# Optimization experiments

Hardware: AMD Instinct MI355X
Metric: run time of the kernel (lower is better)

## Reference

```python
import jax, jax.numpy as jnp
import numpy as np

B, L, D = 2, 4096, 768
H, HD = 12, 64
EPS = 1e-6


def setup_inputs() -> dict:
    key = jax.random.key(0)
    ks = jax.random.split(key, 5)
    x = jax.random.normal(ks[0], (B, L, D), dtype=jnp.float32)
    # realistic rope tables
    inv_freq = 1.0 / (10000.0 ** (np.arange(0, HD, 2, dtype=np.float32) / HD))
    t = np.arange(L, dtype=np.float32)
    freqs = np.outer(t, inv_freq)  # (L, HD/2)
    emb = np.concatenate([freqs, freqs], axis=-1)  # (L, HD)
    rope_cos = jnp.asarray(np.cos(emb))
    rope_sin = jnp.asarray(np.sin(emb))
    Wqkv = jax.random.normal(ks[1], (3 * D, D), dtype=jnp.float32) * (1.0 / np.sqrt(D))
    Wout = jax.random.normal(ks[2], (D, D), dtype=jnp.float32) * (1.0 / np.sqrt(D))
    q_norm_w = jnp.ones((HD,), dtype=jnp.float32)
    k_norm_w = jnp.ones((HD,), dtype=jnp.float32)
    return {"x": x, "rope_cos": rope_cos, "rope_sin": rope_sin,
            "Wqkv": Wqkv, "Wout": Wout,
            "q_norm_w": q_norm_w, "k_norm_w": k_norm_w}


def _rms_norm(x, w):
    # x: (..., HD); computed in float32 like the torch module
    norm = jax.lax.rsqrt(jnp.mean(jnp.square(x.astype(jnp.float32)), axis=-1, keepdims=True) + EPS)
    return (x.astype(jnp.float32) * norm).astype(x.dtype) * w


def _rotate_half(x):
    x1, x2 = jnp.split(x, 2, axis=-1)
    return jnp.concatenate([-x2, x1], axis=-1)


def reference(x, rope_cos, rope_sin, Wqkv, Wout, q_norm_w, k_norm_w):
    b, l, d = x.shape
    # fused QKV projection (Linear with no bias): x @ Wqkv.T
    qkv = jnp.einsum('bld,ed->ble', x, Wqkv).reshape(b, l, 3, H, HD)
    q, k, v = qkv[:, :, 0], qkv[:, :, 1], qkv[:, :, 2]  # (B, L, H, HD)
    q = jnp.transpose(q, (0, 2, 1, 3))  # (B, H, L, HD)
    k = jnp.transpose(k, (0, 2, 1, 3))
    v = jnp.transpose(v, (0, 2, 1, 3))
    # per-head RMSNorm on q and k
    q = _rms_norm(q, q_norm_w)
    k = _rms_norm(k, k_norm_w)
    # RoPE: cos/sin (L, HD) broadcast over (B, H)
    cos = rope_cos[None, None, :, :]
    sin = rope_sin[None, None, :, :]
    q = q * cos + _rotate_half(q) * sin
    k = k * cos + _rotate_half(k) * sin
    # scaled dot product attention (no mask)
    scale = 1.0 / jnp.sqrt(jnp.asarray(HD, dtype=q.dtype))
    scores = jnp.einsum('bhqd,bhkd->bhqk', q, k) * scale  # (B, H, L, L)
    attn = jax.nn.softmax(scores, axis=-1)
    out = jnp.einsum('bhqk,bhkd->bhqd', attn, v)  # (B, H, L, HD)
    out = jnp.transpose(out, (0, 2, 1, 3)).reshape(b, l, d)
    return jnp.einsum('bld,ed->ble', out, Wout)
```

## Files before the change

kernel.cpp:

```cpp
#include <hip/hip_runtime.h>
#include <hip/hip_bf16.h>

typedef float f32x4 __attribute__((ext_vector_type(4)));
typedef float f32x16 __attribute__((ext_vector_type(16)));
typedef short bf16x8 __attribute__((ext_vector_type(8)));
typedef unsigned short ushort8_t __attribute__((ext_vector_type(8)));

#define L_SEQ 4096
#define DMODEL 768
#define NHEAD 12
#define HDIM 64
#define QSCALE (0.125f * 1.44269504f)

__device__ __forceinline__ unsigned short f2bf(float f) {
    __hip_bfloat16 h = __float2bfloat16(f);
    return *reinterpret_cast<unsigned short*>(&h);
}

__device__ __forceinline__ unsigned pack2bf(float a, float b) {
    unsigned r;
    asm("v_cvt_pk_bf16_f32 %0, %1, %2" : "=v"(r) : "v"(a), "v"(b));
    return r;
}

__device__ __forceinline__ void gload16(const void* g, void* l) {
    __builtin_amdgcn_global_load_lds(
        (const __attribute__((address_space(1))) unsigned int*)g,
        (__attribute__((address_space(3))) unsigned int*)l, 16, 0, 0);
}

__global__ __launch_bounds__(256) void cvt3_f32_bf16(
    const float* __restrict__ a, unsigned short* __restrict__ oa, int na,
    const float* __restrict__ bsrc, unsigned short* __restrict__ ob, int nb,
    const float* __restrict__ csrc, unsigned short* __restrict__ oc, int nc)
{
    int i = (blockIdx.x * 256 + threadIdx.x) * 4;
    const float* in; unsigned short* out;
    if (i < na) { in = a; out = oa; }
    else if (i < na + nb) { in = bsrc; out = ob; i -= na; }
    else if (i < na + nb + nc) { in = csrc; out = oc; i -= na + nb; }
    else return;
    float4 v = *reinterpret_cast<const float4*>(in + i);
    ushort4 o;
    o.x = f2bf(v.x); o.y = f2bf(v.y); o.z = f2bf(v.z); o.w = f2bf(v.w);
    *reinterpret_cast<ushort4*>(out + i) = o;
}

#define BM 128
#define BN 128
#define BKK 64

__global__ __launch_bounds__(256) void gemm_qkv_fused(
    const unsigned short* __restrict__ A, const unsigned short* __restrict__ Bt,
    const float* __restrict__ cosb, const float* __restrict__ sinb,
    const float* __restrict__ qw, const float* __restrict__ kw,
    unsigned short* __restrict__ Qb, unsigned short* __restrict__ Kb,
    unsigned short* __restrict__ Vt)
{
    __shared__ union SM {
        struct { unsigned short As[BM][BKK]; unsigned short Bs[BN][BKK]; } st;
        unsigned short ep[4][64][72];
    } sm;

    const int K = DMODEL;
    const int tid  = threadIdx.x;
    const int lane = tid & 63;
    const int wid  = tid >> 6;
    const int r = lane & 15, g = lane >> 4;
    const int wr = wid >> 1, wc = wid & 1;
    const int m0 = blockIdx.y * BM;
    const int n0 = blockIdx.x * BN;

    f32x4 acc[4][4];
    for (int i = 0; i < 4; ++i)
        for (int j = 0; j < 4; ++j)
            acc[i][j] = (f32x4){0.f, 0.f, 0.f, 0.f};

    for (int kt = 0; kt < K; kt += BKK) {
        __syncthreads();
        for (int p = 0; p < 4; ++p) {
            int idx = wid * 64 + p * 256 + lane;
            int row = idx >> 3;
            int ch  = (idx & 7) * 8;
            gload16(&A[(size_t)(m0 + row) * K + kt + ch],
                    (char*)sm.st.As + (size_t)(wid * 64 + p * 256) * 16);
            gload16(&Bt[(size_t)(n0 + row) * K + kt + ch],
                    (char*)sm.st.Bs + (size_t)(wid * 64 + p * 256) * 16);
        }
        __syncthreads();
        for (int k0 = 0; k0 < BKK; k0 += 32) {
            bf16x8 a[4], b[4];
            for (int i = 0; i < 4; ++i)
                a[i] = *reinterpret_cast<const bf16x8*>(&sm.st.As[wr * 64 + i * 16 + r][k0 + 8 * g]);
            for (int j = 0; j < 4; ++j)
                b[j] = *reinterpret_cast<const bf16x8*>(&sm.st.Bs[wc * 64 + j * 16 + r][k0 + 8 * g]);
            for (int i = 0; i < 4; ++i)
                for (int j = 0; j < 4; ++j)
                    acc[i][j] = __builtin_amdgcn_mfma_f32_16x16x32_bf16(a[i], b[j], acc[i][j], 0, 0, 0);
        }
    }

    __syncthreads();

    const int e0  = n0 + wc * 64;
    const int sec = e0 / DMODEL;
    const int h   = (e0 % DMODEL) / HDIM;
    const int row0 = m0 + wr * 64;
    const int b   = row0 >> 12;
    const int l0  = row0 & (L_SEQ - 1);
    unsigned short (*ep)[72] = sm.ep[wid];

    if (sec < 2) {
        const float* nw = (sec == 0) ? qw : kw;
        float wv[4];
        for (int j = 0; j < 4; ++j) wv[j] = nw[j * 16 + r];
        for (int i = 0; i < 4; ++i) {
            for (int t = 0; t < 4; ++t) {
                float ss = acc[i][0][t] * acc[i][0][t] + acc[i][1][t] * acc[i][1][t]
                         + acc[i][2][t] * acc[i][2][t] + acc[i][3][t] * acc[i][3][t];
                ss += __shfl_xor(ss, 1);
                ss += __shfl_xor(ss, 2);
                ss += __shfl_xor(ss, 4);
                ss += __shfl_xor(ss, 8);
                float inv = rsqrtf(ss * (1.f / 64.f) + 1e-6f);
                int lr = i * 16 + 4 * g + t;
                int l  = l0 + lr;
                float qn[4];
                for (int j = 0; j < 4; ++j) qn[j] = acc[i][j][t] * inv * wv[j];
                for (int j = 0; j < 4; ++j) {
                    int d = j * 16 + r;
                    float c = cosb[l * HDIM + d], s = sinb[l * HDIM + d];
                    float sgn = (j < 2) ? -1.f : 1.f;
                    float res = qn[j] * c + sgn * qn[j ^ 2] * s;
                    if (sec == 0) res *= QSCALE;
                    ep[lr][d] = f2bf(res);
                }
            }
        }
        unsigned short* dst = ((sec == 0) ? Qb : Kb)
            + ((size_t)(b * NHEAD + h) * L_SEQ + l0) * HDIM;
        for (int it = 0; it < 8; ++it) {
            int idx = it * 64 + lane;
            int lr = idx >> 3, ch = (idx & 7) * 8;
            ushort8_t v = *reinterpret_cast<const ushort8_t*>(&ep[lr][ch]);
            *reinterpret_cast<ushort8_t*>(&dst[(size_t)lr * HDIM + ch]) = v;
        }
    } else {
        for (int i = 0; i < 4; ++i)
            for (int t = 0; t < 4; ++t) {
                int lr = i * 16 + 4 * g + t;
                for (int j = 0; j < 4; ++j)
                    ep[j * 16 + r][lr] = f2bf(acc[i][j][t]);
            }
        unsigned short* dst = Vt + ((size_t)(b * NHEAD + h) * HDIM) * L_SEQ + l0;
        for (int it = 0; it < 8; ++it) {
            int idx = it * 64 + lane;
            int d = idx >> 3, ch = (idx & 7) * 8;
            ushort8_t v = *reinterpret_cast<const ushort8_t*>(&ep[d][ch]);
            *reinterpret_cast<ushort8_t*>(&dst[(size_t)d * L_SEQ + ch]) = v;
        }
    }
}

__global__ __launch_bounds__(256) void gemm_bf16_nt(
    const unsigned short* __restrict__ A, const unsigned short* __restrict__ Bt,
    float* __restrict__ C, int M, int N, int K)
{
    __shared__ unsigned short As[BM][BKK];
    __shared__ unsigned short Bs[BN][BKK];
    const int tid  = threadIdx.x;
    const int lane = tid & 63;
    const int wid  = tid >> 6;
    const int r = lane & 15, g = lane >> 4;
    const int wr = wid >> 1, wc = wid & 1;
    const int m0 = blockIdx.y * BM;
    const int n0 = blockIdx.x * BN;

    f32x4 acc[4][4];
    for (int i = 0; i < 4; ++i)
        for (int j = 0; j < 4; ++j)
            acc[i][j] = (f32x4){0.f, 0.f, 0.f, 0.f};

    for (int kt = 0; kt < K; kt += BKK) {
        __syncthreads();
        for (int p = 0; p < 4; ++p) {
            int idx = wid * 64 + p * 256 + lane;
            int row = idx >> 3;
            int ch  = (idx & 7) * 8;
            gload16(&A[(size_t)(m0 + row) * K + kt + ch],
                    (char*)As + (size_t)(wid * 64 + p * 256) * 16);
            gload16(&Bt[(size_t)(n0 + row) * K + kt + ch],
                    (char*)Bs + (size_t)(wid * 64 + p * 256) * 16);
        }
        __syncthreads();
        for (int k0 = 0; k0 < BKK; k0 += 32) {
            bf16x8 a[4], b[4];
            for (int i = 0; i < 4; ++i)
                a[i] = *reinterpret_cast<const bf16x8*>(&As[wr * 64 + i * 16 + r][k0 + 8 * g]);
            for (int j = 0; j < 4; ++j)
                b[j] = *reinterpret_cast<const bf16x8*>(&Bs[wc * 64 + j * 16 + r][k0 + 8 * g]);
            for (int i = 0; i < 4; ++i)
                for (int j = 0; j < 4; ++j)
                    acc[i][j] = __builtin_amdgcn_mfma_f32_16x16x32_bf16(a[i], b[j], acc[i][j], 0, 0, 0);
        }
    }
    for (int i = 0; i < 4; ++i)
        for (int j = 0; j < 4; ++j)
            for (int t = 0; t < 4; ++t) {
                int row = m0 + wr * 64 + i * 16 + 4 * g + t;
                int col = n0 + wc * 64 + j * 16 + r;
                C[(size_t)row * N + col] = acc[i][j][t];
            }
}

__global__ __launch_bounds__(256, 3) void flashattn(
    const unsigned short* __restrict__ Qb, const unsigned short* __restrict__ Kb,
    const unsigned short* __restrict__ Vt, unsigned short* __restrict__ aob)
{
    __shared__ unsigned short Ksm[2][64 * 64];
    __shared__ unsigned short Vsm[2][64 * 64];

    const int lin = blockIdx.x;
    const int bh = (lin & 7) + 8 * (lin >> 8);
    const int qblk = (lin >> 3) & 31;
    const int b = bh / NHEAD, h = bh % NHEAD;
    const int tid = threadIdx.x;
    const int wid = tid >> 6, lane = tid & 63;
    const int l31 = lane & 31, half = lane >> 5;
    const int q0 = qblk * 128 + wid * 32;

    bf16x8 qf[4];
    {
        const unsigned short* Qp = Qb + ((size_t)bh * L_SEQ + q0 + l31) * HDIM + 8 * half;
        for (int dt = 0; dt < 4; ++dt)
            qf[dt] = *reinterpret_cast<const bf16x8*>(Qp + dt * 16);
    }

    const unsigned short* Kbase = Kb + (size_t)bh * L_SEQ * HDIM;
    const unsigned short* Vbase = Vt + (size_t)bh * HDIM * L_SEQ;

    const int row0 = tid >> 3;
    const int c0 = ((tid & 7) * 16) ^ ((row0 & 7) << 4);
    const char* kp0 = (const char*)(Kbase + (size_t)row0 * HDIM) + c0;
    const char* vp0 = (const char*)(Vbase + (size_t)row0 * L_SEQ) + c0;

    f32x16 o0, o1, sA0, sA1, sB0, sB1;
    for (int e = 0; e < 16; ++e) {
        o0[e] = 0.f; o1[e] = 0.f;
        sA0[e] = 0.f; sA1[e] = 0.f; sB0[e] = 0.f; sB1[e] = 0.f;
    }
    float lacc = 0.f;

    auto stageK = [&](int buf, int t) {
        size_t off = (size_t)t * (64 * HDIM * 2);
        gload16(kp0 + off, (char*)Ksm[buf] + wid * 1024);
        gload16(kp0 + off + 32 * HDIM * 2, (char*)Ksm[buf] + wid * 1024 + 4096);
    };
    auto stageV = [&](int buf, int t) {
        size_t off = (size_t)t * 128;
        gload16(vp0 + off, (char*)Vsm[buf] + wid * 1024);
        gload16(vp0 + off + (size_t)32 * L_SEQ * 2, (char*)Vsm[buf] + wid * 1024 + 4096);
    };

    auto qk = [&](f32x16& s0, f32x16& s1, const unsigned short* Kbuf) {
        const char* rp0 = (const char*)Kbuf + l31 * 128;
        const char* rp1 = rp0 + 32 * 128;
        const int sw = (l31 & 7) << 4;
        for (int dt = 0; dt < 4; ++dt) {
            int co = (dt * 32 + half * 16) ^ sw;
            bf16x8 kf0 = *reinterpret_cast<const bf16x8*>(rp0 + co);
            bf16x8 kf1 = *reinterpret_cast<const bf16x8*>(rp1 + co);
            s0 = __builtin_amdgcn_mfma_f32_32x32x16_bf16(kf0, qf[dt], s0, 0, 0, 0);
            s1 = __builtin_amdgcn_mfma_f32_32x32x16_bf16(kf1, qf[dt], s1, 0, 0, 0);
        }
    };

    auto softmax_pa = [&](f32x16& s0, f32x16& s1, bf16x8* pa) {
        float ts = 0.f;
        for (int kh = 0; kh < 2; ++kh) {
            f32x16& s = kh ? s1 : s0;
            for (int kk = 0; kk < 2; ++kk) {
                float p8[8];
                for (int e = 0; e < 8; ++e) p8[e] = __builtin_amdgcn_exp2f(s[8 * kk + e]);
                float t0 = (p8[0] + p8[1]) + (p8[2] + p8[3]);
                float t1 = (p8[4] + p8[5]) + (p8[6] + p8[7]);
                ts += t0 + t1;
                unsigned A = pack2bf(p8[0], p8[1]);
                unsigned Bp = pack2bf(p8[2], p8[3]);
                unsigned C = pack2bf(p8[4], p8[5]);
                unsigned D = pack2bf(p8[6], p8[7]);
                asm("v_permlane32_swap_b32 %0, %1" : "+v"(A), "+v"(C));
                asm("v_permlane32_swap_b32 %0, %1" : "+v"(Bp), "+v"(D));
                union { unsigned u[4]; bf16x8 v; } tt;
                tt.u[0] = A; tt.u[1] = Bp; tt.u[2] = C; tt.u[3] = D;
                pa[2 * kh + kk] = tt.v;
            }
            for (int e = 0; e < 16; ++e) s[e] = 0.f;
        }
        lacc += ts;
    };

    auto pv = [&](const bf16x8* pa, const unsigned short* Vbuf) {
        const char* rp0 = (const char*)Vbuf + l31 * 128;
        const char* rp1 = rp0 + 32 * 128;
        const int sw = (l31 & 7) << 4;
        for (int kt = 0; kt < 4; ++kt) {
            int co = (kt * 32 + half * 16) ^ sw;
            bf16x8 vf0 = *reinterpret_cast<const bf16x8*>(rp0 + co);
            bf16x8 vf1 = *reinterpret_cast<const bf16x8*>(rp1 + co);
            o0 = __builtin_amdgcn_mfma_f32_32x32x16_bf16(pa[kt], vf0, o0, 0, 0, 0);
            o1 = __builtin_amdgcn_mfma_f32_32x32x16_bf16(pa[kt], vf1, o1, 0, 0, 0);
        }
    };

    stageK(0, 0);
    __syncthreads();
    stageK(1, 1); stageV(0, 0);
    __builtin_amdgcn_s_setprio(1);
    qk(sA0, sA1, Ksm[0]);
    __builtin_amdgcn_s_setprio(0);
    __syncthreads();

    bf16x8 pa[4];
    for (int i = 0; i < 31; ++i) {
        int t1 = 2 * i + 1;
        stageK(0, t1 + 1); stageV(1, t1);
        __builtin_amdgcn_s_setprio(1);
        qk(sB0, sB1, Ksm[1]);
        softmax_pa(sA0, sA1, pa);
        pv(pa, Vsm[0]);
        __builtin_amdgcn_s_setprio(0);
        __syncthreads();
        int t2 = t1 + 1;
        stageK(1, t2 + 1); stageV(0, t2);
        __builtin_amdgcn_s_setprio(1);
        qk(sA0, sA1, Ksm[0]);
        softmax_pa(sB0, sB1, pa);
        pv(pa, Vsm[1]);
        __builtin_amdgcn_s_setprio(0);
        __syncthreads();
    }
    stageV(1, 63);
    __builtin_amdgcn_s_setprio(1);
    qk(sB0, sB1, Ksm[1]);
    softmax_pa(sA0, sA1, pa);
    pv(pa, Vsm[0]);
    __builtin_amdgcn_s_setprio(0);
    __syncthreads();
    softmax_pa(sB0, sB1, pa);
    pv(pa, Vsm[1]);

    float ltot = lacc + __shfl_xor(lacc, 32);

    for (int j = 0; j < 16; ++j) {
        int q = (j & 3) + 8 * (j >> 2) + 4 * half;
        float linv = 1.f / __shfl(ltot, q);
        size_t base = ((size_t)(b * L_SEQ + q0 + q)) * DMODEL + h * HDIM + l31;
        aob[base] = f2bf(o0[j] * linv);
        aob[base + 32] = f2bf(o1[j] * linv);
    }
}

extern "C" void kernel_launch(void* const* d_in, const int* in_sizes, int n_in,
                              void* d_out, int out_size, void* d_ws, size_t ws_size,
                              hipStream_t stream) {
    const float* x        = (const float*)d_in[0];
    const float* rope_cos = (const float*)d_in[1];
    const float* rope_sin = (const float*)d_in[2];
    const float* Wqkv     = (const float*)d_in[3];
    const float* Wout     = (const float*)d_in[4];
    const float* q_norm_w = (const float*)d_in[5];
    const float* k_norm_w = (const float*)d_in[6];
    float* out = (float*)d_out;

    const int BL = 2 * L_SEQ;
    const int nx    = BL * DMODEL;
    const int nwqkv = 3 * DMODEL * DMODEL;
    const int nwout = DMODEL * DMODEL;

    char* w = (char*)d_ws;
    unsigned short* xb    = (unsigned short*)w; w += (size_t)nx * 2;
    unsigned short* wqkvb = (unsigned short*)w; w += (size_t)nwqkv * 2;
    unsigned short* woutb = (unsigned short*)w; w += (size_t)nwout * 2;
    unsigned short* Qb    = (unsigned short*)w; w += (size_t)nx * 2;
    unsigned short* Kb    = (unsigned short*)w; w += (size_t)nx * 2;
    unsigned short* Vtb   = (unsigned short*)w; w += (size_t)nx * 2;
    unsigned short* aob   = (unsigned short*)w; w += (size_t)nx * 2;

    {
        int total = (nx + nwqkv + nwout) / 4;
        cvt3_f32_bf16<<<(total + 255) / 256, 256, 0, stream>>>(
            x, xb, nx, Wqkv, wqkvb, nwqkv, Wout, woutb, nwout);
    }

    {
        dim3 grid(3 * DMODEL / BN, BL / BM);
        gemm_qkv_fused<<<grid, 256, 0, stream>>>(xb, wqkvb, rope_cos, rope_sin,
                                                 q_norm_w, k_norm_w, Qb, Kb, Vtb);
    }

    flashattn<<<768, 256, 0, stream>>>(Qb, Kb, Vtb, aob);

    {
        dim3 grid(DMODEL / BN, BL / BM);
        gemm_bf16_nt<<<grid, 256, 0, stream>>>(aob, woutb, out, BL, DMODEL, DMODEL);
    }
}
```

Measured before the change: 209.9 us.

## Replace software-pipelined QK/softmax/PV loop with simple double-buffered loop

Removes the cross-iteration software pipeline, in which QK for tile t+1 was computed while softmax and PV of tile t ran, using two sets of score accumulators. It replaces it with a straightforward loop: prefetch K/V for the next tile, then QK, softmax and PV on the current tile. This frees 32 accumulator registers per lane, which could raise occupancy. In exchange it loses the overlap of MFMA work with exp/softmax work inside a wave. The setprio scope also changes so softmax runs at normal priority.

```diff
diff --git a/kernel.cpp b/kernel.cpp
--- a/kernel.cpp
+++ b/kernel.cpp
@@ -244,10 +244,9 @@
     const char* kp0 = (const char*)(Kbase + (size_t)row0 * HDIM) + c0;
     const char* vp0 = (const char*)(Vbase + (size_t)row0 * L_SEQ) + c0;
 
-    f32x16 o0, o1, sA0, sA1, sB0, sB1;
+    f32x16 o0, o1, s0, s1;
     for (int e = 0; e < 16; ++e) {
-        o0[e] = 0.f; o1[e] = 0.f;
-        sA0[e] = 0.f; sA1[e] = 0.f; sB0[e] = 0.f; sB1[e] = 0.f;
+        o0[e] = 0.f; o1[e] = 0.f; s0[e] = 0.f; s1[e] = 0.f;
     }
     float lacc = 0.f;
 
@@ -262,7 +261,7 @@
         gload16(vp0 + off + (size_t)32 * L_SEQ * 2, (char*)Vsm[buf] + wid * 1024 + 4096);
     };
 
-    auto qk = [&](f32x16& s0, f32x16& s1, const unsigned short* Kbuf) {
+    auto qk = [&](const unsigned short* Kbuf) {
         const char* rp0 = (const char*)Kbuf + l31 * 128;
         const char* rp1 = rp0 + 32 * 128;
         const int sw = (l31 & 7) << 4;
@@ -275,16 +274,14 @@
         }
     };
 
-    auto softmax_pa = [&](f32x16& s0, f32x16& s1, bf16x8* pa) {
+    auto softmax_pa = [&](bf16x8* pa) {
         float ts = 0.f;
         for (int kh = 0; kh < 2; ++kh) {
             f32x16& s = kh ? s1 : s0;
             for (int kk = 0; kk < 2; ++kk) {
                 float p8[8];
                 for (int e = 0; e < 8; ++e) p8[e] = __builtin_amdgcn_exp2f(s[8 * kk + e]);
-                float t0 = (p8[0] + p8[1]) + (p8[2] + p8[3]);
-                float t1 = (p8[4] + p8[5]) + (p8[6] + p8[7]);
-                ts += t0 + t1;
+                ts += ((p8[0] + p8[1]) + (p8[2] + p8[3])) + ((p8[4] + p8[5]) + (p8[6] + p8[7]));
                 unsigned A = pack2bf(p8[0], p8[1]);
                 unsigned Bp = pack2bf(p8[2], p8[3]);
                 unsigned C = pack2bf(p8[4], p8[5]);
@@ -313,42 +310,22 @@
         }
     };
 
-    stageK(0, 0);
+    stageK(0, 0); stageV(0, 0);
     __syncthreads();
-    stageK(1, 1); stageV(0, 0);
-    __builtin_amdgcn_s_setprio(1);
-    qk(sA0, sA1, Ksm[0]);
-    __builtin_amdgcn_s_setprio(0);
-    __syncthreads();
 
     bf16x8 pa[4];
-    for (int i = 0; i < 31; ++i) {
-        int t1 = 2 * i + 1;
-        stageK(0, t1 + 1); stageV(1, t1);
+    for (int t = 0; t < 64; ++t) {
+        int cur = t & 1;
+        if (t + 1 < 64) { stageK(cur ^ 1, t + 1); stageV(cur ^ 1, t + 1); }
         __builtin_amdgcn_s_setprio(1);
-        qk(sB0, sB1, Ksm[1]);
-        softmax_pa(sA0, sA1, pa);
-        pv(pa, Vsm[0]);
+        qk(Ksm[cur]);
         __builtin_amdgcn_s_setprio(0);
-        __syncthreads();
-        int t2 = t1 + 1;
-        stageK(1, t2 + 1); stageV(0, t2);
+        softmax_pa(pa);
         __builtin_amdgcn_s_setprio(1);
-        qk(sA0, sA1, Ksm[0]);
-        softmax_pa(sB0, sB1, pa);
-        pv(pa, Vsm[1]);
+        pv(pa, Vsm[cur]);
         __builtin_amdgcn_s_setprio(0);
         __syncthreads();
     }
-    stageV(1, 63);
-    __builtin_amdgcn_s_setprio(1);
-    qk(sB0, sB1, Ksm[1]);
-    softmax_pa(sA0, sA1, pa);
-    pv(pa, Vsm[0]);
-    __builtin_amdgcn_s_setprio(0);
-    __syncthreads();
-    softmax_pa(sB0, sB1, pa);
-    pv(pa, Vsm[1]);
 
     float ltot = lacc + __shfl_xor(lacc, 32);
 
```

Result: slower. 221.2 us (+5.4%).
